# Optimization experiments

Measured on AMD Instinct MI355X. Metric: run time of the kernel, lower is better.

The kernel has to match this reference:

```python
import jax, jax.numpy as jnp
import numpy as np

# Irrep layout of node_vec: 128x0e | 64x1e (64*3) | 32x2e (32*5)
MUL0, MUL1, MUL2 = 128, 64, 32
A = 32  # node_attr scalar channels (32x0e)
N = 8192


def setup_inputs() -> dict:
    key = jax.random.key(0)
    ks = jax.random.split(key, 12)
    f32 = jnp.float32
    return {
        "node_vec": jax.random.normal(ks[0], (N, MUL0 + 3 * MUL1 + 5 * MUL2), f32),
        "node_embedding": jax.random.normal(ks[1], (N, A), f32),
        # fctp_1: TP(input, attr) -> gated irreps (scalars + gates + vectors)
        "W1s": jax.random.normal(ks[2], (MUL0, A, MUL0), f32),          # 0e x 0e -> 0e
        "b1s": jnp.zeros((MUL0,), f32),
        "W1g": jax.random.normal(ks[3], (MUL0, A, MUL1 + MUL2), f32),   # 0e x 0e -> gate 0e
        "b1g": jnp.zeros((MUL1 + MUL2,), f32),
        "W1v1": jax.random.normal(ks[4], (MUL1, A, MUL1), f32),         # 1e x 0e -> 1e
        "W1v2": jax.random.normal(ks[5], (MUL2, A, MUL2), f32),         # 2e x 0e -> 2e
        # fctp_2: TP(mlp_mid, attr) -> 32x0e (only scalar path allowed by CG rules)
        "W2": jax.random.normal(ks[6], (MUL0, A, A), f32),
        "b2": jnp.zeros((A,), f32),
        # output network: LinearRS(32->32) + SiLU + LinearRS(32->1)
        "W3": jax.random.normal(ks[7], (A, A), f32),
        "b3": jnp.zeros((A,), f32),
        "W4": jax.random.normal(ks[8], (A, 1), f32),
        "b4": jnp.zeros((1,), f32),
    }


def reference(node_vec, node_embedding, W1s, b1s, W1g, b1g, W1v1, W1v2, W2, b2, W3, b3, W4, b4):
    n = node_vec.shape[0]
    attr = node_embedding
    # split features by irrep degree
    s = node_vec[:, :MUL0]                                         # [n,128]   0e
    v1 = node_vec[:, MUL0:MUL0 + 3 * MUL1].reshape(n, MUL1, 3)     # [n,64,3]  1e
    v2 = node_vec[:, MUL0 + 3 * MUL1:].reshape(n, MUL2, 5)         # [n,32,5]  2e

    inv = lambda u: 1.0 / np.sqrt(u * A).astype(np.float32)

    # ---- fctp_1: fully-connected TP with scalar attr (l x 0e -> l per-path mixing) ----
    s_mid = jnp.einsum('nu,nv,uvw->nw', s, attr, W1s) * inv(MUL0) + b1s
    g = jnp.einsum('nu,nv,uvw->nw', s, attr, W1g) * inv(MUL0) + b1g
    v1_mid = jnp.einsum('num,nv,uvw->nwm', v1, attr, W1v1) * inv(MUL1)
    v2_mid = jnp.einsum('num,nv,uvw->nwm', v2, attr, W1v2) * inv(MUL2)

    # ---- SwishGate: SiLU on scalars, sigmoid gates on vectors ----
    s_act = jax.nn.silu(s_mid)
    gate = jax.nn.sigmoid(g)
    v1_g = v1_mid * gate[:, :MUL1, None]
    v2_g = v2_mid * gate[:, MUL1:, None]
    # NOTE: v1_g/v2_g have no allowed CG path into the 0e output of fctp_2 (l x 0 -> 0
    # only for l=0), so they do not contribute — exactly as in the original module.
    del v1_g, v2_g

    # ---- fctp_2: mlp_mid x attr -> 32x0e (scalar path only) ----
    h = jnp.einsum('nu,nv,uvw->nw', s_act, attr, W2) * inv(MUL0) + b2

    # ---- output network: LinearRS + SiLU + LinearRS ----
    h = jax.nn.silu(h @ (W3 / np.sqrt(A).astype(np.float32)) + b3)
    pred_energy = h @ (W4 / np.sqrt(A).astype(np.float32)) + b4     # [n,1]
    return pred_energy
```

## Files before the change

kernel.cpp:

```cpp
#include <hip/hip_runtime.h>

typedef _Float16 f16;
typedef f16 f16x8 __attribute__((ext_vector_type(8)));
typedef f16 f16x4 __attribute__((ext_vector_type(4)));
typedef f16 f16x2 __attribute__((ext_vector_type(2)));
typedef float f32x4 __attribute__((ext_vector_type(4)));

union F8 { uint4 u4; f16x8 v; f16x2 h[4]; f16 e[8]; };

__global__ __launch_bounds__(256) void prep_kernel(
    const float* __restrict__ W1s, const float* __restrict__ W2,
    f16* __restrict__ W1P, f16* __restrict__ W2P)
{
    __shared__ f16 T[32 * 36];
    const int b = blockIdx.x, t = threadIdx.x;

    const float* src; f16* dst; int u, w0, W;
    if (b < 512) { u = b >> 2; w0 = (b & 3) * 32; W = 128; src = W1s; dst = W1P; }
    else         { u = b - 512; w0 = 0;           W = 32;  src = W2;  dst = W2P; }
    {
        int v = t >> 3, wq = t & 7;
        float4 f = *(const float4*)(src + (size_t)(u * 32 + v) * W + w0 + wq * 4);
        T[v * 36 + wq * 4 + 0] = (f16)f.x;
        T[v * 36 + wq * 4 + 1] = (f16)f.y;
        T[v * 36 + wq * 4 + 2] = (f16)f.z;
        T[v * 36 + wq * 4 + 3] = (f16)f.w;
    }
    __syncthreads();
    {
        int w = t >> 3, vr = t & 7;
        f16x4 o = { T[(vr * 4 + 0) * 36 + w], T[(vr * 4 + 1) * 36 + w],
                    T[(vr * 4 + 2) * 36 + w], T[(vr * 4 + 3) * 36 + w] };
        *(f16x4*)(dst + (size_t)u * (W * 32) + (size_t)(w0 + w) * 32 + vr * 4) = o;
    }
}

__global__ __launch_bounds__(256, 2) void gemm1_kernel(
    const float* __restrict__ node_vec, const float* __restrict__ attr,
    const f16* __restrict__ W1P, const float* __restrict__ b1s,
    f16* __restrict__ s_act)
{
    __shared__ alignas(16) f16 s_lds[32 * 136];

    const int t  = threadIdx.x;
    const int n0 = blockIdx.x * 32;
    const int l  = t & 63, lr = l & 15, q = l >> 4;
    const int c0 = blockIdx.y * 64 + (t >> 6) * 16;

    #pragma unroll
    for (int i = 0; i < 4; ++i) {
        int idx = t + 256 * i;
        int r = idx >> 5, c4 = idx & 31;
        float4 f = *(const float4*)(node_vec + (size_t)(n0 + r) * 480 + c4 * 4);
        f16x4 o = { (f16)f.x, (f16)f.y, (f16)f.z, (f16)f.w };
        *(f16x4*)(s_lds + r * 136 + c4 * 4) = o;
    }

    F8 af0, af1;
    #pragma unroll
    for (int kk = 0; kk < 4; ++kk) {
        float2 fa = *(const float2*)(attr + (size_t)(n0 + lr) * 32 + q * 8 + kk * 2);
        float2 fb = *(const float2*)(attr + (size_t)(n0 + 16 + lr) * 32 + q * 8 + kk * 2);
        af0.h[kk] = f16x2{ (f16)fa.x, (f16)fa.y };
        af1.h[kk] = f16x2{ (f16)fb.x, (f16)fb.y };
    }

    const f16* Bp = W1P + ((size_t)(c0 + lr)) * 32 + q * 8;
    f16x8 B[8];
    #pragma unroll
    for (int j = 0; j < 8; ++j)
        B[j] = *(const f16x8*)(Bp + (size_t)j * 4096);

    __syncthreads();

    f32x4 acc0 = {0.f, 0.f, 0.f, 0.f}, acc1 = {0.f, 0.f, 0.f, 0.f};

    F8 s8[2][2];
    s8[0][0].v = *(const f16x8*)(s_lds + lr * 136);
    s8[0][1].v = *(const f16x8*)(s_lds + (16 + lr) * 136);

    #pragma unroll
    for (int uo = 0; uo < 16; ++uo) {
        const int cur = uo & 1, nxt = cur ^ 1;
        const int uon = (uo + 1 < 16) ? uo + 1 : 15;
        s8[nxt][0].v = *(const f16x8*)(s_lds + lr * 136 + uon * 8);
        s8[nxt][1].v = *(const f16x8*)(s_lds + (16 + lr) * 136 + uon * 8);
        #pragma unroll
        for (int j = 0; j < 8; ++j) {
            const int u = uo * 8 + j;
            f16x8 bf = B[j];
            const int un = (u + 8 < 128) ? (u + 8) : u;
            B[j] = *(const f16x8*)(Bp + (size_t)un * 4096);
            f16 sv0 = s8[cur][0].e[j];
            f16 sv1 = s8[cur][1].e[j];
            f16x2 sb0 = { sv0, sv0 }, sb1 = { sv1, sv1 };
            F8 a0, a1;
            #pragma unroll
            for (int kk = 0; kk < 4; ++kk) {
                a0.h[kk] = sb0 * af0.h[kk];
                a1.h[kk] = sb1 * af1.h[kk];
            }
            acc0 = __builtin_amdgcn_mfma_f32_16x16x32_f16(a0.v, bf, acc0, 0, 0, 0);
            acc1 = __builtin_amdgcn_mfma_f32_16x16x32_f16(a1.v, bf, acc1, 0, 0, 0);
        }
    }

    const float bv = b1s[c0 + lr];
    #pragma unroll
    for (int reg = 0; reg < 4; ++reg) {
        float v0 = acc0[reg] * 0.015625f + bv;
        float v1 = acc1[reg] * 0.015625f + bv;
        s_act[(size_t)(n0 + q * 4 + reg) * 128 + c0 + lr] =
            (f16)(v0 / (1.f + __expf(-v0)));
        s_act[(size_t)(n0 + 16 + q * 4 + reg) * 128 + c0 + lr] =
            (f16)(v1 / (1.f + __expf(-v1)));
    }
}

__global__ __launch_bounds__(256, 2) void gemm2_head_kernel(
    const f16* __restrict__ s_act, const float* __restrict__ attr,
    const f16* __restrict__ W2P, const float* __restrict__ b2,
    const float* __restrict__ W3, const float* __restrict__ b3,
    const float* __restrict__ W4, const float* __restrict__ b4,
    float* __restrict__ out)
{
    __shared__ alignas(16) f16 s_lds[32 * 136];
    __shared__ alignas(16) float red[4][32 * 36];
    __shared__ alignas(16) float W3_lds[32 * 36];
    __shared__ alignas(16) float h_lds[32 * 36];

    const int t  = threadIdx.x;
    const int n0 = blockIdx.x * 32;
    const int wv = t >> 6, l = t & 63, lr = l & 15, q = l >> 4;
    const int u0 = wv * 32;

    const f16* B2p = W2P + ((size_t)u0 * 32 + lr) * 32 + q * 8;
    f16x8 B0[8], B1[8];
    #pragma unroll
    for (int j = 0; j < 8; ++j) {
        B0[j] = *(const f16x8*)(B2p + (size_t)j * 1024);
        B1[j] = *(const f16x8*)(B2p + (size_t)j * 1024 + 512);
    }

    F8 af0, af1;
    #pragma unroll
    for (int kk = 0; kk < 4; ++kk) {
        float2 fa = *(const float2*)(attr + (size_t)(n0 + lr) * 32 + q * 8 + kk * 2);
        float2 fb = *(const float2*)(attr + (size_t)(n0 + 16 + lr) * 32 + q * 8 + kk * 2);
        af0.h[kk] = f16x2{ (f16)fa.x, (f16)fa.y };
        af1.h[kk] = f16x2{ (f16)fb.x, (f16)fb.y };
    }

    #pragma unroll
    for (int i = 0; i < 2; ++i) {
        int ch = t + 256 * i;
        int r = ch >> 4, c8 = ch & 15;
        *(uint4*)(s_lds + r * 136 + c8 * 8) =
            *(const uint4*)(s_act + (size_t)(n0 + r) * 128 + c8 * 8);
    }
    { int i = t >> 3, jj = (t & 7) * 4;
      *(f32x4*)(W3_lds + i * 36 + jj) = *(const f32x4*)(W3 + i * 32 + jj); }
    __syncthreads();

    f32x4 acc00 = {0,0,0,0}, acc01 = {0,0,0,0};
    f32x4 acc10 = {0,0,0,0}, acc11 = {0,0,0,0};

    F8 s8[2][2];
    s8[0][0].v = *(const f16x8*)(s_lds + lr * 136 + u0);
    s8[0][1].v = *(const f16x8*)(s_lds + (16 + lr) * 136 + u0);

    #pragma unroll
    for (int uo = 0; uo < 4; ++uo) {
        const int cur = uo & 1, nxt = cur ^ 1;
        const int uon = (uo + 1 < 4) ? uo + 1 : 3;
        s8[nxt][0].v = *(const f16x8*)(s_lds + lr * 136 + u0 + uon * 8);
        s8[nxt][1].v = *(const f16x8*)(s_lds + (16 + lr) * 136 + u0 + uon * 8);
        #pragma unroll
        for (int j = 0; j < 8; ++j) {
            const int k = uo * 8 + j;
            f16x8 bf0 = B0[j], bf1 = B1[j];
            const int kn = (k + 8 < 32) ? (k + 8) : k;
            B0[j] = *(const f16x8*)(B2p + (size_t)kn * 1024);
            B1[j] = *(const f16x8*)(B2p + (size_t)kn * 1024 + 512);
            f16 sv0 = s8[cur][0].e[j];
            f16 sv1 = s8[cur][1].e[j];
            f16x2 sb0 = { sv0, sv0 }, sb1 = { sv1, sv1 };
            F8 a0, a1;
            #pragma unroll
            for (int kk = 0; kk < 4; ++kk) {
                a0.h[kk] = sb0 * af0.h[kk];
                a1.h[kk] = sb1 * af1.h[kk];
            }
            acc00 = __builtin_amdgcn_mfma_f32_16x16x32_f16(a0.v, bf0, acc00, 0, 0, 0);
            acc01 = __builtin_amdgcn_mfma_f32_16x16x32_f16(a0.v, bf1, acc01, 0, 0, 0);
            acc10 = __builtin_amdgcn_mfma_f32_16x16x32_f16(a1.v, bf0, acc10, 0, 0, 0);
            acc11 = __builtin_amdgcn_mfma_f32_16x16x32_f16(a1.v, bf1, acc11, 0, 0, 0);
        }
    }

    #pragma unroll
    for (int reg = 0; reg < 4; ++reg) {
        red[wv][(q * 4 + reg) * 36 + lr]           = acc00[reg];
        red[wv][(q * 4 + reg) * 36 + 16 + lr]      = acc01[reg];
        red[wv][(16 + q * 4 + reg) * 36 + lr]      = acc10[reg];
        red[wv][(16 + q * 4 + reg) * 36 + 16 + lr] = acc11[reg];
    }
    __syncthreads();

    {
        int row = t >> 3, c4 = (t & 7) * 4;
        f32x4 s = *(const f32x4*)(&red[0][row * 36 + c4]);
        s = s + *(const f32x4*)(&red[1][row * 36 + c4]);
        s = s + *(const f32x4*)(&red[2][row * 36 + c4]);
        s = s + *(const f32x4*)(&red[3][row * 36 + c4]);
        #pragma unroll
        for (int e = 0; e < 4; ++e)
            h_lds[row * 36 + c4 + e] = s[e] * 0.015625f + b2[c4 + e];
    }
    __syncthreads();

    {
        int node = t >> 3, j4 = (t & 7) * 4;
        float a0 = 0.f, a1 = 0.f, a2 = 0.f, a3 = 0.f;
        #pragma unroll
        for (int i = 0; i < 32; ++i) {
            float hv = h_lds[node * 36 + i];
            a0 += hv * W3_lds[i * 36 + j4 + 0];
            a1 += hv * W3_lds[i * 36 + j4 + 1];
            a2 += hv * W3_lds[i * 36 + j4 + 2];
            a3 += hv * W3_lds[i * 36 + j4 + 3];
        }
        const float inv = 0.17677669529663687f;
        float p = 0.f;
        float aa[4] = { a0, a1, a2, a3 };
        #pragma unroll
        for (int e = 0; e < 4; ++e) {
            float tv = aa[e] * inv + b3[j4 + e];
            float g  = tv / (1.f + __expf(-tv));
            p += g * W4[j4 + e] * inv;
        }
        p += __shfl_xor(p, 1);
        p += __shfl_xor(p, 2);
        p += __shfl_xor(p, 4);
        if ((t & 7) == 0) out[n0 + node] = p + b4[0];
    }
}

extern "C" void kernel_launch(void* const* d_in, const int* in_sizes, int n_in,
                              void* d_out, int out_size, void* d_ws, size_t ws_size,
                              hipStream_t stream)
{
    const float* node_vec = (const float*)d_in[0];
    const float* attr     = (const float*)d_in[1];
    const float* W1s      = (const float*)d_in[2];
    const float* b1s      = (const float*)d_in[3];
    const float* W2       = (const float*)d_in[8];
    const float* b2       = (const float*)d_in[9];
    const float* W3       = (const float*)d_in[10];
    const float* b3       = (const float*)d_in[11];
    const float* W4       = (const float*)d_in[12];
    const float* b4       = (const float*)d_in[13];
    float* out = (float*)d_out;

    char* ws = (char*)d_ws;
    f16* W1P   = (f16*)(ws);
    f16* W2P   = (f16*)(ws + (1u << 20));
    f16* s_act = (f16*)(ws + (1280u << 10));

    prep_kernel<<<640, 256, 0, stream>>>(W1s, W2, W1P, W2P);
    gemm1_kernel<<<dim3(256, 2), 256, 0, stream>>>(node_vec, attr, W1P, b1s, s_act);
    gemm2_head_kernel<<<256, 256, 0, stream>>>(s_act, attr, W2P, b2,
                                               W3, b3, W4, b4, out);
}
```

Measured before the change: 117.0 us.

## Enlarge gemm1 block tile to 64 rows with 2x2 MFMA register tiling per wave

```diff
diff --git a/kernel.cpp b/kernel.cpp
--- a/kernel.cpp
+++ b/kernel.cpp
@@ -40,15 +40,17 @@
     const f16* __restrict__ W1P, const float* __restrict__ b1s,
     f16* __restrict__ s_act)
 {
-    __shared__ alignas(16) f16 s_lds[32 * 136];
+    __shared__ alignas(16) f16 s_lds[64 * 136];
 
     const int t  = threadIdx.x;
-    const int n0 = blockIdx.x * 32;
-    const int l  = t & 63, lr = l & 15, q = l >> 4;
-    const int c0 = blockIdx.y * 64 + (t >> 6) * 16;
-
-    #pragma unroll
-    for (int i = 0; i < 4; ++i) {
+    const int n0 = blockIdx.x * 64;
+    const int wv = t >> 6, l = t & 63, lr = l & 15, q = l >> 4;
+    const int mtp = wv & 1, cs = wv >> 1;
+    const int c0 = blockIdx.y * 64 + cs * 32;
+    const int r0 = 32 * mtp;
+
+    #pragma unroll
+    for (int i = 0; i < 8; ++i) {
         int idx = t + 256 * i;
         int r = idx >> 5, c4 = idx & 31;
         float4 f = *(const float4*)(node_vec + (size_t)(n0 + r) * 480 + c4 * 4);
@@ -59,38 +61,42 @@
     F8 af0, af1;
     #pragma unroll
     for (int kk = 0; kk < 4; ++kk) {
-        float2 fa = *(const float2*)(attr + (size_t)(n0 + lr) * 32 + q * 8 + kk * 2);
-        float2 fb = *(const float2*)(attr + (size_t)(n0 + 16 + lr) * 32 + q * 8 + kk * 2);
+        float2 fa = *(const float2*)(attr + (size_t)(n0 + r0 + lr) * 32 + q * 8 + kk * 2);
+        float2 fb = *(const float2*)(attr + (size_t)(n0 + r0 + 16 + lr) * 32 + q * 8 + kk * 2);
         af0.h[kk] = f16x2{ (f16)fa.x, (f16)fa.y };
         af1.h[kk] = f16x2{ (f16)fb.x, (f16)fb.y };
     }
 
     const f16* Bp = W1P + ((size_t)(c0 + lr)) * 32 + q * 8;
-    f16x8 B[8];
-    #pragma unroll
-    for (int j = 0; j < 8; ++j)
-        B[j] = *(const f16x8*)(Bp + (size_t)j * 4096);
-
-    __syncthreads();
-
-    f32x4 acc0 = {0.f, 0.f, 0.f, 0.f}, acc1 = {0.f, 0.f, 0.f, 0.f};
+    f16x8 B0[8], B1[8];
+    #pragma unroll
+    for (int j = 0; j < 8; ++j) {
+        B0[j] = *(const f16x8*)(Bp + (size_t)j * 4096);
+        B1[j] = *(const f16x8*)(Bp + (size_t)j * 4096 + 512);
+    }
+
+    __syncthreads();
+
+    f32x4 acc00 = {0,0,0,0}, acc01 = {0,0,0,0};
+    f32x4 acc10 = {0,0,0,0}, acc11 = {0,0,0,0};
 
     F8 s8[2][2];
-    s8[0][0].v = *(const f16x8*)(s_lds + lr * 136);
-    s8[0][1].v = *(const f16x8*)(s_lds + (16 + lr) * 136);
+    s8[0][0].v = *(const f16x8*)(s_lds + (r0 + lr) * 136);
+    s8[0][1].v = *(const f16x8*)(s_lds + (r0 + 16 + lr) * 136);
 
     #pragma unroll
     for (int uo = 0; uo < 16; ++uo) {
         const int cur = uo & 1, nxt = cur ^ 1;
         const int uon = (uo + 1 < 16) ? uo + 1 : 15;
-        s8[nxt][0].v = *(const f16x8*)(s_lds + lr * 136 + uon * 8);
-        s8[nxt][1].v = *(const f16x8*)(s_lds + (16 + lr) * 136 + uon * 8);
+        s8[nxt][0].v = *(const f16x8*)(s_lds + (r0 + lr) * 136 + uon * 8);
+        s8[nxt][1].v = *(const f16x8*)(s_lds + (r0 + 16 + lr) * 136 + uon * 8);
         #pragma unroll
         for (int j = 0; j < 8; ++j) {
             const int u = uo * 8 + j;
-            f16x8 bf = B[j];
+            f16x8 bf0 = B0[j], bf1 = B1[j];
             const int un = (u + 8 < 128) ? (u + 8) : u;
-            B[j] = *(const f16x8*)(Bp + (size_t)un * 4096);
+            B0[j] = *(const f16x8*)(Bp + (size_t)un * 4096);
+            B1[j] = *(const f16x8*)(Bp + (size_t)un * 4096 + 512);
             f16 sv0 = s8[cur][0].e[j];
             f16 sv1 = s8[cur][1].e[j];
             f16x2 sb0 = { sv0, sv0 }, sb1 = { sv1, sv1 };
@@ -100,20 +106,27 @@
                 a0.h[kk] = sb0 * af0.h[kk];
                 a1.h[kk] = sb1 * af1.h[kk];
             }
-            acc0 = __builtin_amdgcn_mfma_f32_16x16x32_f16(a0.v, bf, acc0, 0, 0, 0);
-            acc1 = __builtin_amdgcn_mfma_f32_16x16x32_f16(a1.v, bf, acc1, 0, 0, 0);
-        }
-    }
-
-    const float bv = b1s[c0 + lr];
+            acc00 = __builtin_amdgcn_mfma_f32_16x16x32_f16(a0.v, bf0, acc00, 0, 0, 0);
+            acc01 = __builtin_amdgcn_mfma_f32_16x16x32_f16(a0.v, bf1, acc01, 0, 0, 0);
+            acc10 = __builtin_amdgcn_mfma_f32_16x16x32_f16(a1.v, bf0, acc10, 0, 0, 0);
+            acc11 = __builtin_amdgcn_mfma_f32_16x16x32_f16(a1.v, bf1, acc11, 0, 0, 0);
+        }
+    }
+
+    const float bv0 = b1s[c0 + lr];
+    const float bv1 = b1s[c0 + 16 + lr];
     #pragma unroll
     for (int reg = 0; reg < 4; ++reg) {
-        float v0 = acc0[reg] * 0.015625f + bv;
-        float v1 = acc1[reg] * 0.015625f + bv;
-        s_act[(size_t)(n0 + q * 4 + reg) * 128 + c0 + lr] =
-            (f16)(v0 / (1.f + __expf(-v0)));
-        s_act[(size_t)(n0 + 16 + q * 4 + reg) * 128 + c0 + lr] =
-            (f16)(v1 / (1.f + __expf(-v1)));
+        int ra = n0 + r0 + q * 4 + reg;
+        int rb = n0 + r0 + 16 + q * 4 + reg;
+        float v00 = acc00[reg] * 0.015625f + bv0;
+        float v01 = acc01[reg] * 0.015625f + bv1;
+        float v10 = acc10[reg] * 0.015625f + bv0;
+        float v11 = acc11[reg] * 0.015625f + bv1;
+        s_act[(size_t)ra * 128 + c0 + lr]      = (f16)(v00 / (1.f + __expf(-v00)));
+        s_act[(size_t)ra * 128 + c0 + 16 + lr] = (f16)(v01 / (1.f + __expf(-v01)));
+        s_act[(size_t)rb * 128 + c0 + lr]      = (f16)(v10 / (1.f + __expf(-v10)));
+        s_act[(size_t)rb * 128 + c0 + 16 + lr] = (f16)(v11 / (1.f + __expf(-v11)));
     }
 }
 
@@ -268,7 +281,7 @@
     f16* s_act = (f16*)(ws + (1280u << 10));
 
     prep_kernel<<<640, 256, 0, stream>>>(W1s, W2, W1P, W2P);
-    gemm1_kernel<<<dim3(256, 2), 256, 0, stream>>>(node_vec, attr, W1P, b1s, s_act);
+    gemm1_kernel<<<dim3(128, 2), 256, 0, stream>>>(node_vec, attr, W1P, b1s, s_act);
     gemm2_head_kernel<<<256, 256, 0, stream>>>(s_act, attr, W2P, b2,
                                                W3, b3, W4, b4, out);
 }
```

Result: slower. 119.8 us (+2.3%).
